# Optimization experiments

Hardware: AMD Instinct MI355X
Metric: run time of the kernel (lower is better)

The kernel has to match this reference:

```python
import jax, jax.numpy as jnp
from jax import lax
import numpy as np

H = W = 2048
C = 3
KSIZE = 2
SIGMA = 2.0
ITERATIONS = 2
RADII = (256.0, 768.0)
# with max_displacement=0 all circle centers coincide, so 'close to any circle'
# reduces to distance^2 < max(radius^2)
SRADII_MAX = max(r ** 2 for r in RADII)
SCLEAN_MAX = max(max(r - KSIZE, 0.0) ** 2 for r in RADII)


def _gaussian_blur(x, sigma):
    """skimage.filters.gaussian equivalent: separable gaussian, truncate=4.0,
    mode='nearest' (edge padding), channel_axis=-1 (no blur across channels)."""
    radius = int(4.0 * sigma + 0.5)
    t = np.arange(-radius, radius + 1, dtype=np.float32)
    k = np.exp(-0.5 * (t / sigma) ** 2)
    k = (k / k.sum()).astype(np.float32)
    for axis in (0, 1):
        pad = [(0, 0)] * x.ndim
        pad[axis] = (radius, radius)
        xp = jnp.pad(x, pad, mode='edge')
        n = x.shape[axis]
        acc = jnp.zeros_like(x)
        for j in range(k.shape[0]):
            acc = acc + k[j] * lax.slice_in_dim(xp, j, j + n, axis=axis)
        x = acc
    return x


def _glass_forward(img, offsets):
    r = KSIZE
    Hv = H - 2 * r + 1  # loop range(r, H-r+1) -> H-2r+1 rows
    Wv = W - 2 * r + 1
    HWtot = H * W
    # original quirk: cx = shape[0]//2 compared against column index w,
    # cy = shape[1]//2 against row index h; identical for a square image.
    cx = H // 2
    cy = W // 2
    ys = jnp.arange(r, H - r + 1)
    xs = jnp.arange(r, W - r + 1)
    HH, WW = jnp.meshgrid(ys, xs, indexing='ij')  # (Hv, Wv)
    d2 = (cx - WW) ** 2 + (cy - HH) ** 2
    swap_mask = (d2 >= SRADII_MAX).reshape(-1)  # swap only OUTSIDE all circles
    local = ((HH - r) * Wv + (WW - r)).reshape(-1)  # raster order within loop
    lin = (HH * W + WW).reshape(-1)

    # Every read in the original swap loop comes from array_orig (never
    # updated), so the final value of each pixel equals array_orig[source]
    # where source is determined by the LAST write targeting that pixel.
    # Each loop step emits two ordered writes:
    #   array[h, w]   = orig[h_, w_]   (order = 2*raster)
    #   array[h_, w_] = orig[h, w]    (order = 2*raster + 1)
    # We replay this exactly with a scatter-max over write order.
    writes = []
    for i in range(ITERATIONS):
        dh = offsets[i, :, :, 0]
        dw = offsets[i, :, :, 1]
        lin_ = ((HH + dh) * W + (WW + dw)).reshape(-1)
        base = i * 2 * Hv * Wv
        o1 = base + 2 * local
        o2 = o1 + 1
        writes.append((lin, lin_, o1))
        writes.append((lin_, lin, o2))

    win = jnp.full((HWtot,), -1, jnp.int32)
    for tgt, src_idx, order in writes:
        win = win.at[tgt].max(jnp.where(swap_mask, order, -1))
    src = jnp.full((HWtot,), -1, jnp.int32)
    for tgt, src_idx, order in writes:
        hit = swap_mask & (order == win[tgt])
        src = src.at[tgt].max(jnp.where(hit, src_idx, -1))

    orig_flat = img.reshape(HWtot, C)
    gathered = orig_flat[jnp.maximum(src, 0)]
    swapped = jnp.where((src >= 0)[:, None], gathered, orig_flat).reshape(H, W, C)

    blurred = jnp.clip(_gaussian_blur(swapped / 255.0, SIGMA), 0.0, 1.0) * 255.0

    # restore original pixels close to the shrunken (clean) circles
    clean = d2 < SCLEAN_MAX  # (Hv, Wv)
    clean_full = jnp.zeros((H, W), bool).at[r:H - r + 1, r:W - r + 1].set(clean)
    return jnp.where(clean_full[:, :, None], img, blurred)


def setup_inputs() -> dict:
    key = jax.random.key(0)
    k1, k2 = jax.random.split(key)
    img = jax.random.uniform(k1, (H, W, C), jnp.float32) * 255.0
    offsets = jax.random.randint(
        k2, (ITERATIONS, H - 2 * KSIZE + 1, W - 2 * KSIZE + 1, 2),
        -KSIZE, KSIZE, dtype=jnp.int32)
    return {"img": img, "offsets": offsets}


def reference(img, offsets):
    return _glass_forward(img, offsets)
```

## Files before the change

### kernel.cpp

```cpp
#include <hip/hip_runtime.h>
#include <hip/hip_fp16.h>

#define Hh 2048
#define Ww 2048
#define HW (2048 * 2048)
constexpr int REG = 2045;
constexpr int RBASE = 2 * 2045 * 2045;
constexpr int SWAP_D2 = 589824;
constexpr int CLEAN_D2 = 586756;
constexpr int SKIP_D2 = 569000;

__device__ __constant__ float GK[17] = {
    6.691628e-05f, 4.363490e-04f, 2.215963e-03f, 8.764304e-03f,
    2.699596e-02f, 6.475994e-02f, 1.209875e-01f, 1.760358e-01f,
    1.9947466e-01f, 1.760358e-01f, 1.209875e-01f, 6.475994e-02f,
    2.699596e-02f, 8.764304e-03f, 2.215963e-03f, 4.363490e-04f,
    6.691628e-05f};

__device__ __forceinline__ int clampi(int v, int lo, int hi) {
  return v < lo ? lo : (v > hi ? hi : v);
}

constexpr int TX = 32, TY = 8;
constexpr int HX = TX + 3, HY = TY + 3;

__global__ __launch_bounds__(256) void swap_gather(
    const float* __restrict__ img, const int* __restrict__ off,
    __half* __restrict__ A) {
  __shared__ unsigned sh[HY * HX];
  __shared__ __align__(16) float simg[12 * 108];
  int x0 = blockIdx.x * TX, y0 = blockIdx.y * TY;
  int tx = threadIdx.x & 31, ty = threadIdx.x >> 5;
  int px = x0 + tx, py = y0 + ty;
  int plin = py * Ww + px;

  int bxx = max(abs(1024 - x0), abs(1024 - (x0 + TX - 1)));
  int bxy = max(abs(1024 - y0), abs(1024 - (y0 + TY - 1)));
  if (bxx * bxx + bxy * bxy < SKIP_D2) return;

  float r, g, b;
  int mxx = max(abs(1024 - (x0 - 1)), abs(1024 - (x0 + TX + 1)));
  int mxy = max(abs(1024 - (y0 - 1)), abs(1024 - (y0 + TY + 1)));
  if (mxx * mxx + mxy * mxy >= SWAP_D2) {
    for (int e = threadIdx.x; e < HY * HX; e += 256) {
      int ly = e / HX, lx = e - ly * HX;
      int qy = y0 - 1 + ly, qx = x0 - 1 + lx;
      unsigned v = 0xFFFFFFFFu;
      int dcx = 1024 - qx, dcy = 1024 - qy;
      if (qy >= 2 && qy <= 2046 && qx >= 2 && qx <= 2046 &&
          dcx * dcx + dcy * dcy >= SWAP_D2) {
        int base = ((qy - 2) * REG + (qx - 2)) * 2;
        const int2 a0 = *(const int2*)&off[base];
        const int2 a1 = *(const int2*)&off[RBASE + base];
        v = (unsigned)(a0.y + 2) | ((unsigned)(a0.x + 2) << 8) |
            ((unsigned)(a1.y + 2) << 16) | ((unsigned)(a1.x + 2) << 24);
      }
      sh[e] = v;
    }
    if (x0 >= 2 && x0 <= 2013) {
      for (int e = threadIdx.x; e < 648; e += 256) {
        int rr = e / 54, c2 = e - rr * 54;
        int qy = clampi(y0 - 2 + rr, 0, 2047);
        *(float2*)&simg[rr * 108 + 2 * c2] =
            *(const float2*)&img[(size_t)qy * 6144 + (size_t)(x0 - 2) * 3 +
                                 2 * c2];
      }
    } else {
      for (int e = threadIdx.x; e < 1296; e += 256) {
        int rr = e / 108, c3 = e - rr * 108;
        int col = c3 / 3, ch = c3 - col * 3;
        int qy = clampi(y0 - 2 + rr, 0, 2047);
        int qx = clampi(x0 - 2 + col, 0, 2047);
        simg[e] = img[((size_t)qy * Ww + qx) * 3 + ch];
      }
    }
    __syncthreads();

    unsigned w[4][4];
#pragma unroll
    for (int dyi = 0; dyi < 4; ++dyi)
#pragma unroll
      for (int dxi = 0; dxi < 4; ++dxi)
        w[dyi][dxi] = sh[(ty + dyi) * HX + (tx + dxi)];

    int loff = 0;
#define CANDC(dyi, dxi) ((unsigned)((1 - (dxi)) + 2) | ((unsigned)((1 - (dyi)) + 2) << 8))
#define LOFFC(dyi, dxi) (-(1 - (dyi)) * 36 - (1 - (dxi)))
#define CAND0(dyi, dxi) \
  if ((w[dyi][dxi] & 0xFFFFu) == CANDC(dyi, dxi)) loff = LOFFC(dyi, dxi);
#define CAND1(dyi, dxi) \
  if ((w[dyi][dxi] >> 16) == CANDC(dyi, dxi)) loff = LOFFC(dyi, dxi);

    CAND0(0, 0) CAND0(0, 1) CAND0(0, 2) CAND0(0, 3)
    CAND0(1, 0) CAND0(1, 1) CAND0(1, 2) CAND0(1, 3)
    CAND0(2, 0) CAND0(2, 1) CAND0(2, 2) CAND0(2, 3)
    CAND0(3, 0) CAND0(3, 1) CAND0(3, 2) CAND0(3, 3)
    CAND1(0, 0) CAND1(0, 1) CAND1(0, 2) CAND1(0, 3)
    CAND1(1, 0)
    {
      unsigned wc = w[1][1];
      if ((wc >> 24) != 0xFFu) {
        int dh1 = (int)((wc >> 24) & 0xFFu) - 2;
        int dw1 = (int)((wc >> 16) & 0xFFu) - 2;
        loff = dh1 * 36 + dw1;
      }
    }
    CAND1(1, 1) CAND1(1, 2) CAND1(1, 3)
    CAND1(2, 0) CAND1(2, 1) CAND1(2, 2) CAND1(2, 3)
    CAND1(3, 0) CAND1(3, 1) CAND1(3, 2) CAND1(3, 3)
#undef CANDC
#undef LOFFC
#undef CAND0
#undef CAND1

    int L = ((ty + 2) * 36 + (tx + 2) + loff) * 3;
    r = simg[L + 0];
    g = simg[L + 1];
    b = simg[L + 2];
  } else {
    r = img[(size_t)plin * 3 + 0];
    g = img[(size_t)plin * 3 + 1];
    b = img[(size_t)plin * 3 + 2];
  }
  A[plin] = __float2half(r);
  A[HW + plin] = __float2half(g);
  A[2 * HW + plin] = __float2half(b);
}

constexpr int BTW = 128, BTH = 16;
constexpr int SW = BTW + 16;
constexpr int SH = BTH + 16;

__global__ __launch_bounds__(256) void blur_compose(
    const __half* __restrict__ A, const float* __restrict__ img,
    float* __restrict__ out) {
  int lin = blockIdx.x;
  int swz = (lin & 7) * 256 + (lin >> 3);
  int tyb = swz & 127, txb = swz >> 7;
  int x0 = txb * BTW, y0 = tyb * BTH;
  int tid = threadIdx.x;

  int mxx = max(abs(1024 - x0), abs(1024 - (x0 + BTW - 1)));
  int mxy = max(abs(1024 - y0), abs(1024 - (y0 + BTH - 1)));
  if (mxx * mxx + mxy * mxy < CLEAN_D2) {
    const float4* ip = (const float4*)(img + ((size_t)y0 * Ww + x0) * 3);
    float4* op = (float4*)(out + ((size_t)y0 * Ww + x0) * 3);
    for (int e = tid; e < 1536; e += 256) {
      int rr = e / 96, c4 = e - rr * 96;
      op[(size_t)rr * 1536 + c4] = ip[(size_t)rr * 1536 + c4];
    }
    return;
  }

  __shared__ __align__(16) __half S[SH * SW];
  __shared__ __align__(8) __half V[BTH * SW];

  bool xin = (x0 >= 8) && (x0 + SW - 8 <= Ww);

  float br[3][4][2];

  for (int c = 0; c < 3; ++c) {
    const __half* Ap = A + (size_t)c * HW;
    if (xin) {
      for (int e = tid; e < SH * 18; e += 256) {
        int rr = e / 18, ch = e - rr * 18;
        int ys = clampi(y0 - 8 + rr, 0, Hh - 1);
        *(uint4*)&S[rr * SW + ch * 8] =
            *(const uint4*)&Ap[(size_t)ys * Ww + (x0 - 8) + ch * 8];
      }
    } else {
      for (int e = tid; e < SH * SW; e += 256) {
        int rr = e / SW, j = e - rr * SW;
        int ys = clampi(y0 - 8 + rr, 0, Hh - 1);
        int xs = clampi(x0 - 8 + j, 0, Ww - 1);
        S[e] = Ap[(size_t)ys * Ww + xs];
      }
    }
    __syncthreads();
    for (int e = tid; e < BTH * 72; e += 256) {
      int rr = e / 72, p = e - rr * 72;
      float s0 = 0.f, s1 = 0.f;
#pragma unroll
      for (int t = 0; t < 17; ++t) {
        float2 v = __half22float2(*(const __half2*)&S[(rr + t) * SW + 2 * p]);
        s0 += GK[t] * v.x;
        s1 += GK[t] * v.y;
      }
      *(__half2*)&V[rr * SW + 2 * p] = __float22half2_rn(make_float2(s0, s1));
    }
    __syncthreads();
#pragma unroll
    for (int k = 0; k < 4; ++k) {
      int e = tid + (k << 8);
      int rr = e >> 6, x = (e & 63) * 2;
      float f[18];
#pragma unroll
      for (int t = 0; t < 9; ++t) {
        float2 v = __half22float2(*(const __half2*)&V[rr * SW + x + 2 * t]);
        f[2 * t] = v.x;
        f[2 * t + 1] = v.y;
      }
      float s0 = 0.f, s1 = 0.f;
#pragma unroll
      for (int t = 0; t < 17; ++t) {
        s0 += GK[t] * f[t];
        s1 += GK[t] * f[t + 1];
      }
      br[c][k][0] = s0;
      br[c][k][1] = s1;
    }
  }

#pragma unroll
  for (int k = 0; k < 4; ++k) {
    int e = tid + (k << 8);
    int rr = e >> 6, xh = e & 63;
    int y = y0 + rr;
    int xg = x0 + 2 * xh;
    int dy = 1024 - y;
    int dy2 = dy * dy;
    float px[6];
#pragma unroll
    for (int u = 0; u < 2; ++u) {
      int xu = xg + u;
      int dx = 1024 - xu;
      bool clean = (xu >= 2 && xu <= 2046 && y >= 2 && y <= 2046 &&
                    dx * dx + dy2 < CLEAN_D2);
      int p3 = (y * Ww + xu) * 3;
      if (clean) {
        px[3 * u + 0] = img[p3 + 0];
        px[3 * u + 1] = img[p3 + 1];
        px[3 * u + 2] = img[p3 + 2];
      } else {
#pragma unroll
        for (int cc = 0; cc < 3; ++cc) {
          float v = br[cc][k][u];
          v = v < 0.f ? 0.f : (v > 255.f ? 255.f : v);
          px[3 * u + cc] = v;
        }
      }
    }
    float* ob = out + (size_t)(y * Ww + xg) * 3;
    *(float2*)&ob[0] = make_float2(px[0], px[1]);
    *(float2*)&ob[2] = make_float2(px[2], px[3]);
    *(float2*)&ob[4] = make_float2(px[4], px[5]);
  }
}

extern "C" void kernel_launch(void* const* d_in, const int* in_sizes, int n_in,
                              void* d_out, int out_size, void* d_ws,
                              size_t ws_size, hipStream_t stream) {
  const float* img = (const float*)d_in[0];
  const int* off = (const int*)d_in[1];
  float* out = (float*)d_out;

  __half* A = (__half*)d_ws;

  swap_gather<<<dim3(Ww / TX, Hh / TY), 256, 0, stream>>>(img, off, A);
  blur_compose<<<2048, 256, 0, stream>>>(A, img, out);
}
```

Before: 194.6 us.

## Reorder blur blocks heavy-first and register-block vertical blur pass

Block scheduling now uses precomputed tables so all blur-heavy tiles are dispatched first, interleaved across XCDs, and the clean copy-only tiles run last. This is meant to reduce tail imbalance. The vertical blur pass now has each thread compute 4 output rows from 20 loaded inputs, cutting redundant shared-memory reads. The intermediate is kept in fp32 rather than fp16, which doubles the size of that shared buffer. The tables hardcode the tile counts for this image size and circle radius.

```diff
diff --git a/kernel.cpp b/kernel.cpp
--- a/kernel.cpp
+++ b/kernel.cpp
@@ -131,18 +131,44 @@
 constexpr int SW = BTW + 16;
 constexpr int SH = BTH + 16;
 
+__device__ __constant__ short HPRE[17] = {0,   128, 256, 384, 460,  518,
+                                          564, 602, 636, 670, 708,  754,
+                                          812, 888, 1016, 1144, 1272};
+__device__ __constant__ short CPRE[17] = {0,   0,   0,   0,   52,  122,
+                                          204, 294, 388, 482, 572, 654,
+                                          724, 776, 776, 776, 776};
+__device__ __constant__ short CLO[16] = {128, 128, 128, 38, 29, 23, 19, 17,
+                                         17,  19,  23,  29, 38, 128, 128, 128};
+__device__ __constant__ short CCN[16] = {0,  0,  0,  52, 70, 82, 90, 94,
+                                         94, 90, 82, 70, 52, 0,  0,  0};
+constexpr int NHEAVY = 1272;
+constexpr int NCLEAN = 776;
+
 __global__ __launch_bounds__(256) void blur_compose(
     const __half* __restrict__ A, const float* __restrict__ img,
     float* __restrict__ out) {
   int lin = blockIdx.x;
-  int swz = (lin & 7) * 256 + (lin >> 3);
-  int tyb = swz & 127, txb = swz >> 7;
+  int tid = threadIdx.x;
+  int txb, tyb;
+  bool is_clean = lin >= NHEAVY;
+  if (!is_clean) {
+    int idx = (lin & 7) * 159 + (lin >> 3);
+    int c = 0;
+    while (idx >= HPRE[c + 1]) ++c;
+    int j = idx - HPRE[c];
+    txb = c;
+    tyb = j < CLO[c] ? j : j + CCN[c];
+  } else {
+    int l = lin - NHEAVY;
+    int idx = (l & 7) * 97 + (l >> 3);
+    int c = 0;
+    while (idx >= CPRE[c + 1]) ++c;
+    txb = c;
+    tyb = CLO[c] + (idx - CPRE[c]);
+  }
   int x0 = txb * BTW, y0 = tyb * BTH;
-  int tid = threadIdx.x;
-
-  int mxx = max(abs(1024 - x0), abs(1024 - (x0 + BTW - 1)));
-  int mxy = max(abs(1024 - y0), abs(1024 - (y0 + BTH - 1)));
-  if (mxx * mxx + mxy * mxy < CLEAN_D2) {
+
+  if (is_clean) {
     const float4* ip = (const float4*)(img + ((size_t)y0 * Ww + x0) * 3);
     float4* op = (float4*)(out + ((size_t)y0 * Ww + x0) * 3);
     for (int e = tid; e < 1536; e += 256) {
@@ -153,7 +179,7 @@
   }
 
   __shared__ __align__(16) __half S[SH * SW];
-  __shared__ __align__(8) __half V[BTH * SW];
+  __shared__ __align__(8) float Vf[BTH * SW];
 
   bool xin = (x0 >= 8) && (x0 + SW - 8 <= Ww);
 
@@ -177,16 +203,27 @@
       }
     }
     __syncthreads();
-    for (int e = tid; e < BTH * 72; e += 256) {
-      int rr = e / 72, p = e - rr * 72;
-      float s0 = 0.f, s1 = 0.f;
-#pragma unroll
-      for (int t = 0; t < 17; ++t) {
-        float2 v = __half22float2(*(const __half2*)&S[(rr + t) * SW + 2 * p]);
-        s0 += GK[t] * v.x;
-        s1 += GK[t] * v.y;
-      }
-      *(__half2*)&V[rr * SW + 2 * p] = __float22half2_rn(make_float2(s0, s1));
+    for (int e = tid; e < 288; e += 256) {
+      int g = e / 72, p = e - g * 72;
+      int R = g * 4;
+      float2 acc[4] = {make_float2(0.f, 0.f), make_float2(0.f, 0.f),
+                       make_float2(0.f, 0.f), make_float2(0.f, 0.f)};
+#pragma unroll
+      for (int q = 0; q < 20; ++q) {
+        float2 v = __half22float2(*(const __half2*)&S[(R + q) * SW + 2 * p]);
+#pragma unroll
+        for (int k = 0; k < 4; ++k) {
+          int t = q - k;
+          if (t >= 0 && t < 17) {
+            float gk = GK[t];
+            acc[k].x += gk * v.x;
+            acc[k].y += gk * v.y;
+          }
+        }
+      }
+#pragma unroll
+      for (int k = 0; k < 4; ++k)
+        *(float2*)&Vf[(R + k) * SW + 2 * p] = acc[k];
     }
     __syncthreads();
 #pragma unroll
@@ -196,7 +233,7 @@
       float f[18];
 #pragma unroll
       for (int t = 0; t < 9; ++t) {
-        float2 v = __half22float2(*(const __half2*)&V[rr * SW + x + 2 * t]);
+        float2 v = *(const float2*)&Vf[rr * SW + x + 2 * t];
         f[2 * t] = v.x;
         f[2 * t + 1] = v.y;
       }
@@ -257,5 +294,5 @@
   __half* A = (__half*)d_ws;
 
   swap_gather<<<dim3(Ww / TX, Hh / TY), 256, 0, stream>>>(img, off, A);
-  blur_compose<<<2048, 256, 0, stream>>>(A, img, out);
-}
+  blur_compose<<<NHEAVY + NCLEAN, 256, 0, stream>>>(A, img, out);
+}
```

Measured after the change: 231.0 us. 1.19x slower.
